# Kernel tuning notes

Hardware: AMD Instinct MI355X
Metric: run time of the kernel (lower is better)

## Reference

```python
import jax, jax.numpy as jnp
import numpy as np

THETA = 10000.0
EMBED_DIM = 384
NUM_HEADS = 6

def apply_rope_2d(x):
    # x: [B, C, H, W]
    B, C, H, W = x.shape
    dim = C // 2
    inv = 1.0 / THETA ** (jnp.arange(0, dim, 2, dtype=x.dtype) / dim)  # [dim/2]
    fh = jnp.arange(H, dtype=x.dtype)[:, None] * inv[None, :]          # [H, dim/2]
    fw = jnp.arange(W, dtype=x.dtype)[:, None] * inv[None, :]          # [W, dim/2]
    fh_flat = jnp.broadcast_to(fh[:, None, :], (H, W, dim // 2)).reshape(H * W, dim // 2)
    fw_flat = jnp.broadcast_to(fw[None, :, :], (H, W, dim // 2)).reshape(H * W, dim // 2)
    x_seq = x.reshape(B, C, H * W).transpose(0, 2, 1)  # [B, HW, C]
    x_h, x_w = x_seq[..., :dim], x_seq[..., dim:]

    def apply_rotary(t, f):
        # torch stack([c,c],-1).flatten(-2) == repeat each elem twice consecutively
        cos = jnp.repeat(jnp.cos(f), 2, axis=-1)  # [HW, dim]
        sin = jnp.repeat(jnp.sin(f), 2, axis=-1)
        t1, t2 = jnp.split(t, 2, axis=-1)
        rot = jnp.concatenate([-t2, t1], axis=-1)
        return t * cos + rot * sin

    x_h = apply_rotary(x_h, fh_flat)
    x_w = apply_rotary(x_w, fw_flat)
    x_out = jnp.concatenate([x_h, x_w], axis=-1)       # [B, HW, C]
    return x_out.transpose(0, 2, 1).reshape(B, C, H, W)

def conv1x1(x, W, b):
    # 1x1 conv == channel matmul
    return jnp.einsum('oc,bchw->bohw', W, x) + b[None, :, None, None]

def setup_inputs() -> dict:
    key = jax.random.key(0)
    ks = jax.random.split(key, 9)
    B, C, H, W = 8, EMBED_DIM, 64, 64
    s = 1.0 / np.sqrt(C)
    inp = {'x': jax.random.normal(ks[0], (B, C, H, W), dtype=jnp.float32)}
    for i, name in enumerate(['q', 'k', 'v', 'fc']):
        inp[f'W{name}'] = jax.random.uniform(ks[1 + 2 * i], (C, C), dtype=jnp.float32, minval=-s, maxval=s)
        inp[f'b{name}'] = jax.random.uniform(ks[2 + 2 * i], (C,), dtype=jnp.float32, minval=-s, maxval=s)
    return inp

def reference(x, Wq, bq, Wk, bk, Wv, bv, Wfc, bfc):
    B, C, H, W = x.shape
    nh = NUM_HEADS
    hd = C // nh
    scale = hd ** -0.5
    q = apply_rope_2d(conv1x1(x, Wq, bq))
    k = apply_rope_2d(conv1x1(x, Wk, bk))
    v = conv1x1(x, Wv, bv)
    # [B, nh, HW, hd]
    def to_heads(t):
        return t.reshape(B, nh, hd, H * W).transpose(0, 1, 3, 2)
    q = jax.nn.elu(to_heads(q) * scale) + 1.0
    k = jax.nn.elu(to_heads(k)) + 1.0
    v = to_heads(v)
    kv = jnp.einsum('bhnd,bhne->bhde', k, v)               # [B, nh, hd, hd]
    k_sum = k.sum(axis=2)                                   # [B, nh, hd]
    normalizer = jnp.einsum('bhnd,bhd->bhn', q, k_sum)[..., None]
    out = jnp.einsum('bhnd,bhde->bhne', q, kv) / (normalizer + 1e-6)
    out = out.transpose(0, 1, 3, 2).reshape(B, C, H, W)
    return conv1x1(out, Wfc, bfc)
```

## Files before the change

### kernel.cpp

```cpp
#include <hip/hip_runtime.h>
#include <math.h>

#define BATCH 8
#define CCH 384
#define NPIX 4096
#define NHEADS 6
#define SZ ((size_t)BATCH * CCH * NPIX)

typedef __attribute__((ext_vector_type(8))) short short8;
typedef __attribute__((ext_vector_type(4))) float f32x4;

__device__ __forceinline__ float elu1(float x) { return x > 0.f ? x + 1.f : expf(x); }

__device__ __forceinline__ unsigned short bf16_rne(float f) {
    unsigned u = __builtin_bit_cast(unsigned, f);
    u += 0x7FFFu + ((u >> 16) & 1u);
    return (unsigned short)(u >> 16);
}
__device__ __forceinline__ float bf16_f(unsigned short h) {
    return __builtin_bit_cast(float, ((unsigned)h) << 16);
}
__device__ __forceinline__ unsigned packsplit(float v) {
    unsigned short hi = bf16_rne(v);
    unsigned short lo = bf16_rne(v - bf16_f(hi));
    return ((unsigned)hi << 16) | (unsigned)lo;
}

__global__ __launch_bounds__(256) void pack_x_kernel(
    const float* __restrict__ X, unsigned* __restrict__ Xp)
{
    size_t i = ((size_t)blockIdx.x * 256 + threadIdx.x) * 4;
    float4 v = *(const float4*)(X + i);
    uint4 o;
    o.x = packsplit(v.x); o.y = packsplit(v.y);
    o.z = packsplit(v.z); o.w = packsplit(v.w);
    *(uint4*)(Xp + i) = o;
}

__global__ __launch_bounds__(256) void trig_kernel(float2* __restrict__ T)
{
    const float KC = 0.13841367062030680f;
    int idx = blockIdx.x * 256 + threadIdx.x;
    int f = idx >> 6, pos = idx & 63;
    float ang = (float)pos * exp2f(-KC * (float)f);
    float s, c;
    sincosf(ang, &s, &c);
    T[idx] = make_float2(s, c);
}

__global__ __launch_bounds__(256) void pack_w_kernel(
    const float* __restrict__ Wq, const float* __restrict__ Wk,
    const float* __restrict__ Wv, const float* __restrict__ Wfc,
    unsigned short* __restrict__ Wp)
{
    const int tid = threadIdx.x;
    const int lane = tid & 63;
    const int f = blockIdx.x * 4 + (tid >> 6);
    const int rloc = lane & 15;
    const int ks = (lane >> 4) * 8;

    const float* Wsel;
    int ch;
    if (f < 72) {
        int which = f / 24;
        int r = (f % 24) * 16 + rloc;
        if (which < 2) {
            int u = r >> 1;
            int cu = (u < 96) ? u : u + 96;
            ch = cu + 96 * (r & 1);
        } else {
            ch = r;
        }
        Wsel = (which == 0) ? Wq : (which == 1) ? Wk : Wv;
    } else {
        ch = (f - 72) * 16 + rloc;
        Wsel = Wfc;
    }

    for (int c = 0; c < 12; ++c) {
        short8 hv, lv;
#pragma unroll
        for (int j = 0; j < 8; ++j) {
            float v = Wsel[(size_t)ch * CCH + c * 32 + ks + j];
            unsigned short h = bf16_rne(v);
            hv[j] = (short)h;
            lv[j] = (short)bf16_rne(v - bf16_f(h));
        }
        size_t off = (size_t)f * 12288 + (size_t)c * 1024 + (size_t)lane * 8;
        *(short8*)(Wp + off) = hv;
        *(short8*)(Wp + off + 512) = lv;
    }
}

template <int MODE>
__device__ __forceinline__ void gemm_body(
    const unsigned* __restrict__ Xin,
    const unsigned short* __restrict__ Wp,
    const float2* __restrict__ Ttab,
    const float* __restrict__ b0, const float* __restrict__ b1, const float* __restrict__ b2,
    float* __restrict__ O0, float* __restrict__ O1, float* __restrict__ O2)
{
    __shared__ unsigned Bs[32 * 128];

    const int tid = threadIdx.x;
    const int lane = tid & 63;
    const int wv = tid >> 6;
    const int wm = wv >> 1, wn = wv & 1;
    const int mt = blockIdx.y * 2 + wm;
    const int nblk = blockIdx.x;
    const int b = blockIdx.z;
    const int g = lane >> 4;
    const int ln = lane & 15;

    f32x4 acc[4][4] = {};

    const unsigned short* wbase = Wp + (size_t)(mt * 4) * 12288 + (size_t)lane * 8;
    const unsigned* sbU = Xin + (size_t)b * CCH * NPIX + nblk * 128;

    const int r_lo = (lane >> 5);

#pragma unroll 1
    for (int c = 0; c < 12; ++c) {
        __syncthreads();
#pragma unroll
        for (int t = 0; t < 4; ++t) {
            const int r = wv * 8 + t * 2 + r_lo;
            const int P = (r & 7) ^ (((r >> 3) & 1) << 2);
            const int cg = (lane & 31) ^ P;
            const unsigned* gsrc = sbU + (size_t)(c * 32 + r) * NPIX + 4 * cg;
            unsigned* ldst = &Bs[wv * 1024 + t * 256];
            __builtin_amdgcn_global_load_lds(
                (const __attribute__((address_space(1))) unsigned*)gsrc,
                (__attribute__((address_space(3))) unsigned*)ldst, 16, 0, 0);
        }
        __syncthreads();

        short8 ah[4], al[4];
#pragma unroll
        for (int i = 0; i < 4; ++i) {
            const unsigned short* p = wbase + (size_t)i * 12288 + c * 1024;
            ah[i] = *(const short8*)(p);
            al[i] = *(const short8*)(p + 512);
        }

#pragma unroll
        for (int jj = 0; jj < 4; ++jj) {
            const int colbase = wn * 64 + jj * 16 + ln;
            const int cg2 = colbase >> 2;
            const int cw = colbase & 3;
            short8 bh, bl;
#pragma unroll
            for (int j = 0; j < 8; ++j) {
                const int k = g * 8 + j;
                const int Pk = j ^ ((g & 1) << 2);
                unsigned uu = Bs[k * 128 + ((cg2 ^ Pk) << 2) + cw];
                bh[j] = (short)(uu >> 16);
                bl[j] = (short)(uu & 0xFFFFu);
            }
#pragma unroll
            for (int i = 0; i < 4; ++i) {
                acc[i][jj] = __builtin_amdgcn_mfma_f32_16x16x32_bf16(ah[i], bh, acc[i][jj], 0, 0, 0);
                acc[i][jj] = __builtin_amdgcn_mfma_f32_16x16x32_bf16(ah[i], bl, acc[i][jj], 0, 0, 0);
                acc[i][jj] = __builtin_amdgcn_mfma_f32_16x16x32_bf16(al[i], bh, acc[i][jj], 0, 0, 0);
            }
        }
    }

    const int ncol0 = nblk * 128 + wn * 64 + ln;

    if (MODE == 1) {
#pragma unroll
        for (int i = 0; i < 4; ++i) {
            const int rowb = mt * 64 + i * 16 + g * 4;
#pragma unroll
            for (int r = 0; r < 4; ++r) {
                const int row = rowb + r;
                const float bias = b0[row];
                float* orow = O0 + ((size_t)b * CCH + row) * NPIX;
#pragma unroll
                for (int jj = 0; jj < 4; ++jj)
                    orow[ncol0 + jj * 16] = acc[i][jj][r] + bias;
            }
        }
    } else {
        const int which = mt / 6;
        const int mloc = (mt % 6) * 64;
        const float* bsel = (which == 0) ? b0 : (which == 1) ? b1 : b2;
        float* osel = (which == 0) ? O0 : (which == 1) ? O1 : O2;
        if (which == 2) {
#pragma unroll
            for (int i = 0; i < 4; ++i) {
                const int rowb = mloc + i * 16 + g * 4;
#pragma unroll
                for (int r = 0; r < 4; ++r) {
                    const int row = rowb + r;
                    const float bias = bsel[row];
                    float* orow = osel + ((size_t)b * CCH + row) * NPIX;
#pragma unroll
                    for (int jj = 0; jj < 4; ++jj)
                        orow[ncol0 + jj * 16] = acc[i][jj][r] + bias;
                }
            }
        } else {
            const float qs = (which == 0) ? 0.125f : 1.0f;
            const int posH = nblk * 2 + wn;
#pragma unroll
            for (int i = 0; i < 4; ++i) {
#pragma unroll
                for (int p = 0; p < 2; ++p) {
                    const int re = mloc + i * 16 + g * 4 + 2 * p;
                    const int u = re >> 1;
                    const bool isH = (u < 96);
                    const int cu = isH ? u : u + 96;
                    const int jA = isH ? (u >> 1) : ((u - 96) >> 1);
                    const float be = bsel[cu];
                    const float bo = bsel[cu + 96];
                    float* orE = osel + ((size_t)b * CCH + cu) * NPIX;
                    float* orO = orE + (size_t)96 * NPIX;
                    const float2* Ta = Ttab + jA * 64;
                    const float2* Tb = Ttab + (jA + 48) * 64;
                    if (isH) {
                        const float2 fa = Ta[posH];
                        const float2 fb = Tb[posH];
#pragma unroll
                        for (int jj = 0; jj < 4; ++jj) {
                            const int n = ncol0 + jj * 16;
                            const float te = acc[i][jj][2 * p] + be;
                            const float to = acc[i][jj][2 * p + 1] + bo;
                            orE[n] = elu1((te * fa.y - to * fa.x) * qs);
                            orO[n] = elu1((to * fb.y + te * fb.x) * qs);
                        }
                    } else {
#pragma unroll
                        for (int jj = 0; jj < 4; ++jj) {
                            const int n = ncol0 + jj * 16;
                            const int pw = jj * 16 + ln;
                            const float2 fa = Ta[pw];
                            const float2 fb = Tb[pw];
                            const float te = acc[i][jj][2 * p] + be;
                            const float to = acc[i][jj][2 * p + 1] + bo;
                            orE[n] = elu1((te * fa.y - to * fa.x) * qs);
                            orO[n] = elu1((to * fb.y + te * fb.x) * qs);
                        }
                    }
                }
            }
        }
    }
}

__global__ __launch_bounds__(256, 2) void qkv_gemm(
    const unsigned* __restrict__ Xin, const unsigned short* __restrict__ Wp,
    const float2* __restrict__ Ttab,
    const float* __restrict__ b0, const float* __restrict__ b1, const float* __restrict__ b2,
    float* __restrict__ O0, float* __restrict__ O1, float* __restrict__ O2)
{
    gemm_body<0>(Xin, Wp, Ttab, b0, b1, b2, O0, O1, O2);
}

__global__ __launch_bounds__(256, 2) void fc_gemm(
    const unsigned* __restrict__ Xin, const unsigned short* __restrict__ Wp,
    const float2* __restrict__ Ttab,
    const float* __restrict__ b0,
    float* __restrict__ O0)
{
    gemm_body<1>(Xin, Wp, Ttab, b0, b0, b0, O0, O0, O0);
}

__global__ __launch_bounds__(256) void kv_kernel(
    const float* __restrict__ Kin, const float* __restrict__ Vin,
    float* __restrict__ KV, float* __restrict__ KS)
{
    __shared__ float Ks[32][68];
    __shared__ float Vs[32][68];
    const int tid = threadIdx.x;
    const int bh = blockIdx.x;
    const int ns = blockIdx.y;
    const int b = bh / NHEADS, h = bh % NHEADS;
    const float* kb = Kin + ((size_t)b * CCH + h * 64) * NPIX;
    const float* vb = Vin + ((size_t)b * CCH + h * 64) * NPIX;
    const int drow = tid >> 2;
    const int nl = (tid & 3) * 8;
    const int td = (tid & 15) * 4;
    const int te = (tid >> 4) * 4;

    float acc[4][4];
    float ks[4] = {0.f, 0.f, 0.f, 0.f};
#pragma unroll
    for (int i = 0; i < 4; ++i)
#pragma unroll
        for (int j = 0; j < 4; ++j) acc[i][j] = 0.f;

    for (int n0 = ns * 256; n0 < ns * 256 + 256; n0 += 32) {
        __syncthreads();
        const float* kr = kb + (size_t)drow * NPIX + n0 + nl;
        const float* vr = vb + (size_t)drow * NPIX + n0 + nl;
        float4 k0 = *(const float4*)kr;
        float4 k1 = *(const float4*)(kr + 4);
        float4 v0 = *(const float4*)vr;
        float4 v1 = *(const float4*)(vr + 4);
        Ks[nl + 0][drow] = k0.x; Ks[nl + 1][drow] = k0.y;
        Ks[nl + 2][drow] = k0.z; Ks[nl + 3][drow] = k0.w;
        Ks[nl + 4][drow] = k1.x; Ks[nl + 5][drow] = k1.y;
        Ks[nl + 6][drow] = k1.z; Ks[nl + 7][drow] = k1.w;
        Vs[nl + 0][drow] = v0.x; Vs[nl + 1][drow] = v0.y;
        Vs[nl + 2][drow] = v0.z; Vs[nl + 3][drow] = v0.w;
        Vs[nl + 4][drow] = v1.x; Vs[nl + 5][drow] = v1.y;
        Vs[nl + 6][drow] = v1.z; Vs[nl + 7][drow] = v1.w;
        __syncthreads();
#pragma unroll 8
        for (int nn = 0; nn < 32; ++nn) {
            float4 a = *(const float4*)&Ks[nn][td];
            float4 w = *(const float4*)&Vs[nn][te];
            float av[4] = {a.x, a.y, a.z, a.w};
            float wv2[4] = {w.x, w.y, w.z, w.w};
            ks[0] += av[0]; ks[1] += av[1]; ks[2] += av[2]; ks[3] += av[3];
#pragma unroll
            for (int i = 0; i < 4; ++i)
#pragma unroll
                for (int j = 0; j < 4; ++j) acc[i][j] += av[i] * wv2[j];
        }
    }

    float* kvb = KV + (size_t)bh * 64 * 64;
#pragma unroll
    for (int i = 0; i < 4; ++i)
#pragma unroll
        for (int j = 0; j < 4; ++j)
            atomicAdd(&kvb[(td + i) * 64 + (te + j)], acc[i][j]);
    if (te == 0) {
#pragma unroll
        for (int i = 0; i < 4; ++i) atomicAdd(&KS[bh * 64 + td + i], ks[i]);
    }
}

__global__ __launch_bounds__(256) void attn_kernel(
    const float* __restrict__ Q, const float* __restrict__ KV,
    const float* __restrict__ KS, unsigned* __restrict__ O)
{
    __shared__ float Qs[64][132];
    __shared__ float KVs[64][64];
    __shared__ float KSs[64];
    const int tid = threadIdx.x;
    const int n0 = blockIdx.x * 128;
    const int bh = blockIdx.y;
    const int b = bh / NHEADS, h = bh % NHEADS;
    const float* qb = Q + ((size_t)b * CCH + h * 64) * NPIX;

    {
        const int row = tid >> 2;
        const int c0 = (tid & 3) * 32;
        const float* qr = qb + (size_t)row * NPIX + n0 + c0;
#pragma unroll
        for (int j = 0; j < 8; ++j)
            *(float4*)&Qs[row][c0 + j * 4] = *(const float4*)&qr[j * 4];
        const int kc = (tid & 3) * 16;
        const float* kvr = KV + (size_t)bh * 4096 + (size_t)row * 64 + kc;
#pragma unroll
        for (int j = 0; j < 4; ++j)
            *(float4*)&KVs[row][kc + j * 4] = *(const float4*)&kvr[j * 4];
        if (tid < 64) KSs[tid] = KS[bh * 64 + tid];
    }
    __syncthreads();

    const int tx = tid & 31;
    const int ty = tid >> 5;
    float acc[8][4];
    float accn[4] = {0.f, 0.f, 0.f, 0.f};
#pragma unroll
    for (int r = 0; r < 8; ++r)
#pragma unroll
        for (int j = 0; j < 4; ++j) acc[r][j] = 0.f;

#pragma unroll 8
    for (int d = 0; d < 64; ++d) {
        float4 qv = *(const float4*)&Qs[d][tx * 4];
        float qa[4] = {qv.x, qv.y, qv.z, qv.w};
        float ksv = KSs[d];
#pragma unroll
        for (int j = 0; j < 4; ++j) accn[j] += ksv * qa[j];
        float4 k0 = *(const float4*)&KVs[d][ty * 8];
        float4 k1 = *(const float4*)&KVs[d][ty * 8 + 4];
        float kva[8] = {k0.x, k0.y, k0.z, k0.w, k1.x, k1.y, k1.z, k1.w};
#pragma unroll
        for (int r = 0; r < 8; ++r)
#pragma unroll
            for (int j = 0; j < 4; ++j) acc[r][j] += kva[r] * qa[j];
    }

    float rcp[4];
#pragma unroll
    for (int j = 0; j < 4; ++j) rcp[j] = 1.f / (accn[j] + 1e-6f);
#pragma unroll
    for (int r = 0; r < 8; ++r) {
        unsigned* orow = O + ((size_t)b * CCH + h * 64 + ty * 8 + r) * NPIX + n0 + tx * 4;
        uint4 o4;
        o4.x = packsplit(acc[r][0] * rcp[0]);
        o4.y = packsplit(acc[r][1] * rcp[1]);
        o4.z = packsplit(acc[r][2] * rcp[2]);
        o4.w = packsplit(acc[r][3] * rcp[3]);
        *(uint4*)orow = o4;
    }
}

__global__ void zero_kernel(float* p, int n)
{
    int i = blockIdx.x * blockDim.x + threadIdx.x;
    if (i < n) p[i] = 0.f;
}

extern "C" void kernel_launch(void* const* d_in, const int* in_sizes, int n_in,
                              void* d_out, int out_size, void* d_ws, size_t ws_size,
                              hipStream_t stream)
{
    const float* x   = (const float*)d_in[0];
    const float* Wq  = (const float*)d_in[1];
    const float* bq  = (const float*)d_in[2];
    const float* Wk  = (const float*)d_in[3];
    const float* bk  = (const float*)d_in[4];
    const float* Wv  = (const float*)d_in[5];
    const float* bv  = (const float*)d_in[6];
    const float* Wfc = (const float*)d_in[7];
    const float* bfc = (const float*)d_in[8];
    float* out = (float*)d_out;
    float* ws = (float*)d_ws;

    float* q    = ws;
    float* k    = ws + SZ;
    float* v    = ws + 2 * SZ;
    float* kv   = ws + 3 * SZ;
    float* ksum = kv + 48 * 64 * 64;
    float2* Ttab = (float2*)(ksum + 48 * 64);
    unsigned short* Wp = (unsigned short*)(Ttab + 96 * 64);
    unsigned* xp = (unsigned*)d_out;
    unsigned* op = (unsigned*)k;

    const int nz = 48 * 64 * 64 + 48 * 64;
    zero_kernel<<<(nz + 255) / 256, 256, 0, stream>>>(kv, nz);
    trig_kernel<<<24, 256, 0, stream>>>(Ttab);
    pack_w_kernel<<<24, 256, 0, stream>>>(Wq, Wk, Wv, Wfc, Wp);
    pack_x_kernel<<<(int)(SZ / 1024), 256, 0, stream>>>(x, xp);
    qkv_gemm<<<dim3(32, 9, BATCH), 256, 0, stream>>>(xp, Wp, Ttab, bq, bk, bv, q, k, v);
    kv_kernel<<<dim3(48, 16), 256, 0, stream>>>(k, v, kv, ksum);
    attn_kernel<<<dim3(32, 48), 256, 0, stream>>>(q, kv, ksum, op);
    fc_gemm<<<dim3(32, 3, BATCH), 256, 0, stream>>>(op, Wp + (size_t)72 * 12288, Ttab,
                                                    bfc, out);
}
```

Baseline: 353.2 us.

## Double-buffer GEMM LDS staging and move kv reduction to split-bf16 MFMA

The shared GEMM body now double-buffers the LDS tile, so the next K-chunk's global-to-LDS loads are issued while the current chunk is being computed, removing one barrier per iteration. The QKV GEMM epilogue writes K and V already packed as hi/lo bf16 pairs. The kv kernel is rewritten to consume these with three-pass bf16 MFMA instead of scalar FP32 FMAs. KV partials are reduced in LDS before global atomics, with half as many blocks along N. This doubles LDS use in the GEMM and relies on split-bf16 keeping enough precision.

```diff
diff --git a/kernel.cpp b/kernel.cpp
--- a/kernel.cpp
+++ b/kernel.cpp
@@ -24,6 +24,10 @@
     unsigned short hi = bf16_rne(v);
     unsigned short lo = bf16_rne(v - bf16_f(hi));
     return ((unsigned)hi << 16) | (unsigned)lo;
+}
+__device__ __forceinline__ float unpackf(unsigned u) {
+    return __builtin_bit_cast(float, u & 0xFFFF0000u) +
+           __builtin_bit_cast(float, u << 16);
 }
 
 __global__ __launch_bounds__(256) void pack_x_kernel(
@@ -98,9 +102,10 @@
     const unsigned short* __restrict__ Wp,
     const float2* __restrict__ Ttab,
     const float* __restrict__ b0, const float* __restrict__ b1, const float* __restrict__ b2,
-    float* __restrict__ O0, float* __restrict__ O1, float* __restrict__ O2)
-{
-    __shared__ unsigned Bs[32 * 128];
+    float* __restrict__ Oq, unsigned* __restrict__ Ok, unsigned* __restrict__ Ov,
+    float* __restrict__ Ofc)
+{
+    __shared__ unsigned Bs[2][32 * 128];
 
     const int tid = threadIdx.x;
     const int lane = tid & 63;
@@ -116,24 +121,29 @@
 
     const unsigned short* wbase = Wp + (size_t)(mt * 4) * 12288 + (size_t)lane * 8;
     const unsigned* sbU = Xin + (size_t)b * CCH * NPIX + nblk * 128;
-
     const int r_lo = (lane >> 5);
 
-#pragma unroll 1
-    for (int c = 0; c < 12; ++c) {
-        __syncthreads();
+    auto stage = [&](int c, int buf) {
 #pragma unroll
         for (int t = 0; t < 4; ++t) {
             const int r = wv * 8 + t * 2 + r_lo;
             const int P = (r & 7) ^ (((r >> 3) & 1) << 2);
             const int cg = (lane & 31) ^ P;
             const unsigned* gsrc = sbU + (size_t)(c * 32 + r) * NPIX + 4 * cg;
-            unsigned* ldst = &Bs[wv * 1024 + t * 256];
+            unsigned* ldst = &Bs[buf][wv * 1024 + t * 256];
             __builtin_amdgcn_global_load_lds(
                 (const __attribute__((address_space(1))) unsigned*)gsrc,
                 (__attribute__((address_space(3))) unsigned*)ldst, 16, 0, 0);
         }
+    };
+
+    stage(0, 0);
+
+#pragma unroll 1
+    for (int c = 0; c < 12; ++c) {
         __syncthreads();
+        if (c < 11) stage(c + 1, (c + 1) & 1);
+        const unsigned* Bcur = &Bs[c & 1][0];
 
         short8 ah[4], al[4];
 #pragma unroll
@@ -153,7 +163,7 @@
             for (int j = 0; j < 8; ++j) {
                 const int k = g * 8 + j;
                 const int Pk = j ^ ((g & 1) << 2);
-                unsigned uu = Bs[k * 128 + ((cg2 ^ Pk) << 2) + cw];
+                unsigned uu = Bcur[k * 128 + ((cg2 ^ Pk) << 2) + cw];
                 bh[j] = (short)(uu >> 16);
                 bl[j] = (short)(uu & 0xFFFFu);
             }
@@ -176,7 +186,7 @@
             for (int r = 0; r < 4; ++r) {
                 const int row = rowb + r;
                 const float bias = b0[row];
-                float* orow = O0 + ((size_t)b * CCH + row) * NPIX;
+                float* orow = Ofc + ((size_t)b * CCH + row) * NPIX;
 #pragma unroll
                 for (int jj = 0; jj < 4; ++jj)
                     orow[ncol0 + jj * 16] = acc[i][jj][r] + bias;
@@ -186,7 +196,6 @@
         const int which = mt / 6;
         const int mloc = (mt % 6) * 64;
         const float* bsel = (which == 0) ? b0 : (which == 1) ? b1 : b2;
-        float* osel = (which == 0) ? O0 : (which == 1) ? O1 : O2;
         if (which == 2) {
 #pragma unroll
             for (int i = 0; i < 4; ++i) {
@@ -195,14 +204,13 @@
                 for (int r = 0; r < 4; ++r) {
                     const int row = rowb + r;
                     const float bias = bsel[row];
-                    float* orow = osel + ((size_t)b * CCH + row) * NPIX;
+                    unsigned* orow = Ov + ((size_t)b * CCH + row) * NPIX;
 #pragma unroll
                     for (int jj = 0; jj < 4; ++jj)
-                        orow[ncol0 + jj * 16] = acc[i][jj][r] + bias;
+                        orow[ncol0 + jj * 16] = packsplit(acc[i][jj][r] + bias);
                 }
             }
         } else {
-            const float qs = (which == 0) ? 0.125f : 1.0f;
             const int posH = nblk * 2 + wn;
 #pragma unroll
             for (int i = 0; i < 4; ++i) {
@@ -215,32 +223,26 @@
                     const int jA = isH ? (u >> 1) : ((u - 96) >> 1);
                     const float be = bsel[cu];
                     const float bo = bsel[cu + 96];
-                    float* orE = osel + ((size_t)b * CCH + cu) * NPIX;
-                    float* orO = orE + (size_t)96 * NPIX;
+                    const size_t offE = ((size_t)b * CCH + cu) * NPIX;
+                    const size_t offO = offE + (size_t)96 * NPIX;
                     const float2* Ta = Ttab + jA * 64;
                     const float2* Tb = Ttab + (jA + 48) * 64;
-                    if (isH) {
-                        const float2 fa = Ta[posH];
-                        const float2 fb = Tb[posH];
-#pragma unroll
-                        for (int jj = 0; jj < 4; ++jj) {
-                            const int n = ncol0 + jj * 16;
-                            const float te = acc[i][jj][2 * p] + be;
-                            const float to = acc[i][jj][2 * p + 1] + bo;
-                            orE[n] = elu1((te * fa.y - to * fa.x) * qs);
-                            orO[n] = elu1((to * fb.y + te * fb.x) * qs);
-                        }
-                    } else {
-#pragma unroll
-                        for (int jj = 0; jj < 4; ++jj) {
-                            const int n = ncol0 + jj * 16;
-                            const int pw = jj * 16 + ln;
-                            const float2 fa = Ta[pw];
-                            const float2 fb = Tb[pw];
-                            const float te = acc[i][jj][2 * p] + be;
-                            const float to = acc[i][jj][2 * p + 1] + bo;
-                            orE[n] = elu1((te * fa.y - to * fa.x) * qs);
-                            orO[n] = elu1((to * fb.y + te * fb.x) * qs);
+#pragma unroll
+                    for (int jj = 0; jj < 4; ++jj) {
+                        const int n = ncol0 + jj * 16;
+                        const int pw = isH ? posH : (jj * 16 + ln);
+                        const float2 fa = Ta[pw];
+                        const float2 fb = Tb[pw];
+                        const float te = acc[i][jj][2 * p] + be;
+                        const float to = acc[i][jj][2 * p + 1] + bo;
+                        const float ve = te * fa.y - to * fa.x;
+                        const float vo = to * fb.y + te * fb.x;
+                        if (which == 0) {
+                            Oq[offE + n] = elu1(ve * 0.125f);
+                            Oq[offO + n] = elu1(vo * 0.125f);
+                        } else {
+                            Ok[offE + n] = packsplit(elu1(ve));
+                            Ok[offO + n] = packsplit(elu1(vo));
                         }
                     }
                 }
@@ -253,85 +255,96 @@
     const unsigned* __restrict__ Xin, const unsigned short* __restrict__ Wp,
     const float2* __restrict__ Ttab,
     const float* __restrict__ b0, const float* __restrict__ b1, const float* __restrict__ b2,
-    float* __restrict__ O0, float* __restrict__ O1, float* __restrict__ O2)
-{
-    gemm_body<0>(Xin, Wp, Ttab, b0, b1, b2, O0, O1, O2);
+    float* __restrict__ Oq, unsigned* __restrict__ Ok, unsigned* __restrict__ Ov)
+{
+    gemm_body<0>(Xin, Wp, Ttab, b0, b1, b2, Oq, Ok, Ov, nullptr);
 }
 
 __global__ __launch_bounds__(256, 2) void fc_gemm(
     const unsigned* __restrict__ Xin, const unsigned short* __restrict__ Wp,
     const float2* __restrict__ Ttab,
-    const float* __restrict__ b0,
-    float* __restrict__ O0)
-{
-    gemm_body<1>(Xin, Wp, Ttab, b0, b0, b0, O0, O0, O0);
+    const float* __restrict__ b0, float* __restrict__ Ofc)
+{
+    gemm_body<1>(Xin, Wp, Ttab, b0, b0, b0, nullptr, nullptr, nullptr, Ofc);
 }
 
 __global__ __launch_bounds__(256) void kv_kernel(
-    const float* __restrict__ Kin, const float* __restrict__ Vin,
+    const unsigned* __restrict__ Kp, const unsigned* __restrict__ Vp,
     float* __restrict__ KV, float* __restrict__ KS)
 {
-    __shared__ float Ks[32][68];
-    __shared__ float Vs[32][68];
+    __shared__ float red[4096];
     const int tid = threadIdx.x;
+    const int lane = tid & 63;
+    const int wv = tid >> 6;
     const int bh = blockIdx.x;
-    const int ns = blockIdx.y;
     const int b = bh / NHEADS, h = bh % NHEADS;
-    const float* kb = Kin + ((size_t)b * CCH + h * 64) * NPIX;
-    const float* vb = Vin + ((size_t)b * CCH + h * 64) * NPIX;
-    const int drow = tid >> 2;
-    const int nl = (tid & 3) * 8;
-    const int td = (tid & 15) * 4;
-    const int te = (tid >> 4) * 4;
-
-    float acc[4][4];
-    float ks[4] = {0.f, 0.f, 0.f, 0.f};
+    const int ln = lane & 15, g = lane >> 4;
+    const int n0 = blockIdx.y * 512 + wv * 128;
+
+    const unsigned* kb = Kp + ((size_t)b * CCH + h * 64) * NPIX + n0 + g * 8;
+    const unsigned* vb = Vp + ((size_t)b * CCH + h * 64) * NPIX + n0 + g * 8;
+
+    for (int t = tid; t < 4096; t += 256) red[t] = 0.f;
+
+    f32x4 acc[4][4] = {};
+    float ksl[4] = {0.f, 0.f, 0.f, 0.f};
+
+#pragma unroll 1
+    for (int s = 0; s < 4; ++s) {
+        short8 kh[4], kl[4];
+#pragma unroll
+        for (int i = 0; i < 4; ++i) {
+            const unsigned* src = kb + (size_t)(i * 16 + ln) * NPIX + s * 32;
+            uint4 a0 = *(const uint4*)src;
+            uint4 a1 = *(const uint4*)(src + 4);
+            unsigned uu[8] = {a0.x, a0.y, a0.z, a0.w, a1.x, a1.y, a1.z, a1.w};
+#pragma unroll
+            for (int j = 0; j < 8; ++j) {
+                kh[i][j] = (short)(uu[j] >> 16);
+                kl[i][j] = (short)(uu[j] & 0xFFFFu);
+                ksl[i] += unpackf(uu[j]);
+            }
+        }
+#pragma unroll
+        for (int j4 = 0; j4 < 4; ++j4) {
+            const unsigned* src = vb + (size_t)(j4 * 16 + ln) * NPIX + s * 32;
+            uint4 a0 = *(const uint4*)src;
+            uint4 a1 = *(const uint4*)(src + 4);
+            unsigned uu[8] = {a0.x, a0.y, a0.z, a0.w, a1.x, a1.y, a1.z, a1.w};
+            short8 vh, vl;
+#pragma unroll
+            for (int j = 0; j < 8; ++j) {
+                vh[j] = (short)(uu[j] >> 16);
+                vl[j] = (short)(uu[j] & 0xFFFFu);
+            }
+#pragma unroll
+            for (int i = 0; i < 4; ++i) {
+                acc[i][j4] = __builtin_amdgcn_mfma_f32_16x16x32_bf16(kh[i], vh, acc[i][j4], 0, 0, 0);
+                acc[i][j4] = __builtin_amdgcn_mfma_f32_16x16x32_bf16(kh[i], vl, acc[i][j4], 0, 0, 0);
+                acc[i][j4] = __builtin_amdgcn_mfma_f32_16x16x32_bf16(kl[i], vh, acc[i][j4], 0, 0, 0);
+            }
+        }
+    }
+
+#pragma unroll
+    for (int i = 0; i < 4; ++i) {
+        float v2 = ksl[i];
+        v2 += __shfl_xor(v2, 16);
+        v2 += __shfl_xor(v2, 32);
+        if (g == 0) atomicAdd(&KS[bh * 64 + i * 16 + ln], v2);
+    }
+
+    __syncthreads();
 #pragma unroll
     for (int i = 0; i < 4; ++i)
 #pragma unroll
-        for (int j = 0; j < 4; ++j) acc[i][j] = 0.f;
-
-    for (int n0 = ns * 256; n0 < ns * 256 + 256; n0 += 32) {
-        __syncthreads();
-        const float* kr = kb + (size_t)drow * NPIX + n0 + nl;
-        const float* vr = vb + (size_t)drow * NPIX + n0 + nl;
-        float4 k0 = *(const float4*)kr;
-        float4 k1 = *(const float4*)(kr + 4);
-        float4 v0 = *(const float4*)vr;
-        float4 v1 = *(const float4*)(vr + 4);
-        Ks[nl + 0][drow] = k0.x; Ks[nl + 1][drow] = k0.y;
-        Ks[nl + 2][drow] = k0.z; Ks[nl + 3][drow] = k0.w;
-        Ks[nl + 4][drow] = k1.x; Ks[nl + 5][drow] = k1.y;
-        Ks[nl + 6][drow] = k1.z; Ks[nl + 7][drow] = k1.w;
-        Vs[nl + 0][drow] = v0.x; Vs[nl + 1][drow] = v0.y;
-        Vs[nl + 2][drow] = v0.z; Vs[nl + 3][drow] = v0.w;
-        Vs[nl + 4][drow] = v1.x; Vs[nl + 5][drow] = v1.y;
-        Vs[nl + 6][drow] = v1.z; Vs[nl + 7][drow] = v1.w;
-        __syncthreads();
-#pragma unroll 8
-        for (int nn = 0; nn < 32; ++nn) {
-            float4 a = *(const float4*)&Ks[nn][td];
-            float4 w = *(const float4*)&Vs[nn][te];
-            float av[4] = {a.x, a.y, a.z, a.w};
-            float wv2[4] = {w.x, w.y, w.z, w.w};
-            ks[0] += av[0]; ks[1] += av[1]; ks[2] += av[2]; ks[3] += av[3];
-#pragma unroll
-            for (int i = 0; i < 4; ++i)
-#pragma unroll
-                for (int j = 0; j < 4; ++j) acc[i][j] += av[i] * wv2[j];
-        }
-    }
-
-    float* kvb = KV + (size_t)bh * 64 * 64;
-#pragma unroll
-    for (int i = 0; i < 4; ++i)
-#pragma unroll
-        for (int j = 0; j < 4; ++j)
-            atomicAdd(&kvb[(td + i) * 64 + (te + j)], acc[i][j]);
-    if (te == 0) {
-#pragma unroll
-        for (int i = 0; i < 4; ++i) atomicAdd(&KS[bh * 64 + td + i], ks[i]);
-    }
+        for (int j4 = 0; j4 < 4; ++j4)
+#pragma unroll
+            for (int r = 0; r < 4; ++r)
+                atomicAdd(&red[(i * 16 + g * 4 + r) * 64 + j4 * 16 + ln], acc[i][j4][r]);
+    __syncthreads();
+    float* kvb = KV + (size_t)bh * 4096;
+    for (int t = tid; t < 4096; t += 256) atomicAdd(&kvb[t], red[t]);
 }
 
 __global__ __launch_bounds__(256) void attn_kernel(
@@ -425,23 +438,23 @@
     float* out = (float*)d_out;
     float* ws = (float*)d_ws;
 
-    float* q    = ws;
-    float* k    = ws + SZ;
-    float* v    = ws + 2 * SZ;
-    float* kv   = ws + 3 * SZ;
-    float* ksum = kv + 48 * 64 * 64;
+    float*    q  = ws;
+    unsigned* kp = (unsigned*)(ws + SZ);
+    unsigned* vp = (unsigned*)(ws + 2 * SZ);
+    float* kv    = ws + 3 * SZ;
+    float* ksum  = kv + 48 * 64 * 64;
     float2* Ttab = (float2*)(ksum + 48 * 64);
     unsigned short* Wp = (unsigned short*)(Ttab + 96 * 64);
     unsigned* xp = (unsigned*)d_out;
-    unsigned* op = (unsigned*)k;
+    unsigned* op = kp;
 
     const int nz = 48 * 64 * 64 + 48 * 64;
     zero_kernel<<<(nz + 255) / 256, 256, 0, stream>>>(kv, nz);
     trig_kernel<<<24, 256, 0, stream>>>(Ttab);
     pack_w_kernel<<<24, 256, 0, stream>>>(Wq, Wk, Wv, Wfc, Wp);
     pack_x_kernel<<<(int)(SZ / 1024), 256, 0, stream>>>(x, xp);
-    qkv_gemm<<<dim3(32, 9, BATCH), 256, 0, stream>>>(xp, Wp, Ttab, bq, bk, bv, q, k, v);
-    kv_kernel<<<dim3(48, 16), 256, 0, stream>>>(k, v, kv, ksum);
+    qkv_gemm<<<dim3(32, 9, BATCH), 256, 0, stream>>>(xp, Wp, Ttab, bq, bk, bv, q, kp, vp);
+    kv_kernel<<<dim3(48, 8), 256, 0, stream>>>(kp, vp, kv, ksum);
     attn_kernel<<<dim3(32, 48), 256, 0, stream>>>(q, kv, ksum, op);
     fc_gemm<<<dim3(32, 3, BATCH), 256, 0, stream>>>(op, Wp + (size_t)72 * 12288, Ttab,
                                                     bfc, out);
```

Result: slower. 367.4 us (+4.0%).
